# Kernel optimization log

Measured on AMD Instinct MI355X. Metric: run time of the kernel, lower is better.

## Reference

```python
import jax, jax.numpy as jnp
import numpy as np

B, S, IN, OUT = 8, 2048, 4096, 4096
SPARSE_FRACTION = 0.9
ALPHA = 0.3


def setup_inputs() -> dict:
    key = jax.random.key(0)
    k1, k2, k3 = jax.random.split(key, 3)
    total = IN * OUT
    target_nz = int(total * (1.0 - SPARSE_FRACTION))          # nonzeros after rigl step
    num_drop = int(ALPHA * target_nz)                          # = mask.sum() - target_nz
    # kaiming_uniform_(a=sqrt(5)) -> bound = 1/sqrt(fan_in)
    bound = 1.0 / np.sqrt(IN)
    weight = jax.random.uniform(k1, (OUT, IN), minval=-bound, maxval=bound, dtype=jnp.float32)
    x = jax.random.normal(k2, (B, S, IN), dtype=jnp.float32)
    dense_grad = jax.random.normal(k3, (OUT, IN), dtype=jnp.float32) * 0.01
    # mask starts with target_nz + num_drop nonzeros so the drop/grow path runs
    rng = np.random.default_rng(0)
    idx = rng.permutation(total)[: target_nz + num_drop]
    m = np.zeros(total, dtype=bool)
    m[idx] = True
    mask = jnp.asarray(m.reshape(OUT, IN))
    return {"x": x, "weight": weight, "dense_grad": dense_grad, "mask": mask, "num_drop": num_drop}


def _rigl_mask(weight, dense_grad, mask, num_drop):
    # RigL sparse-to-sparse update: drop smallest-|w|, grow largest-|grad| among masked-out slots.
    flat = mask.reshape(-1)
    if num_drop > 0:  # num_drop is a static Python int
        wmag = jnp.abs(weight).reshape(-1)
        _, drop_idx = jax.lax.top_k(-wmag, num_drop)           # smallest magnitudes
        flat = flat.at[drop_idx].set(False)
        gmag = jnp.abs(dense_grad).reshape(-1)
        grow_scores = jnp.where(flat, -jnp.inf, gmag)          # only grow where mask == 0
        _, grow_idx = jax.lax.top_k(grow_scores, num_drop)
        flat = flat.at[grow_idx].set(True)
    return flat.reshape(mask.shape)


def reference(x, weight, dense_grad, mask, num_drop):
    new_mask = _rigl_mask(weight, dense_grad, mask, num_drop)
    masked_weight = weight * new_mask.astype(weight.dtype)     # [OUT, IN]
    # F.linear: y = x @ W^T
    return jnp.einsum('bsi,oi->bso', x, masked_weight)
```

## Files before the change

### kernel.cpp

```cpp
#include <hip/hip_runtime.h>
#include <hip/hip_bf16.h>

#define M_TOT 16384
#define N_TOT 4096
#define K_TOT 4096
#define NELEM 16777216

typedef __attribute__((ext_vector_type(8))) short bf16x8;
typedef __attribute__((ext_vector_type(4))) float f32x4;

#define AS1 __attribute__((address_space(1)))
#define AS3 __attribute__((address_space(3)))

struct SelState {
  unsigned long long prefix;
  unsigned long long thr;
  unsigned int k_rem;
  unsigned int done;
  unsigned int active;
};

struct Ctl {
  unsigned long long pcount;
  unsigned int mask_is_byte;
  unsigned int cand_n;
  SelState d;
  SelState g;
};

__device__ Ctl g_ctl;
__device__ unsigned int g_hist[4096];
__device__ unsigned char g_elig[NELEM];
__device__ unsigned short g_wb[NELEM];
__device__ unsigned short g_xb[(size_t)M_TOT * K_TOT];
__device__ unsigned long long g_cand[NELEM];

__device__ __forceinline__ unsigned short f2bf(float f) {
  unsigned int u = __float_as_uint(f);
  unsigned int r = (u + 0x7FFFu + ((u >> 16) & 1u)) >> 16;
  return (unsigned short)r;
}

__device__ __forceinline__ unsigned long long key_drop_bits(unsigned int fb, int i) {
  unsigned int b = fb & 0x7FFFFFFFu;
  return (((unsigned long long)b) << 24) | (unsigned int)i;
}
__device__ __forceinline__ unsigned long long key_grow_bits(unsigned int fb, int i) {
  unsigned int b = ~(fb & 0x7FFFFFFFu);
  return (((unsigned long long)b) << 24) | (unsigned int)i;
}

__global__ void ctl_reset() {
  int t = threadIdx.x;
  if (t == 0) { g_ctl.pcount = 0ull; g_ctl.cand_n = 0u; }
  for (int i = t; i < 4096; i += 256) g_hist[i] = 0;
}

__global__ void mask_popcnt(const unsigned int* mw) {
  const int NW = NELEM / 4;
  unsigned int s = 0;
  for (int i = blockIdx.x * blockDim.x + threadIdx.x; i < NW; i += gridDim.x * blockDim.x)
    s += __popc(mw[i]);
  for (int off = 32; off > 0; off >>= 1) s += __shfl_down(s, off, 64);
  if ((threadIdx.x & 63) == 0)
    atomicAdd((unsigned long long*)&g_ctl.pcount, (unsigned long long)s);
}

__global__ void sel_init(const int* ndp) {
  unsigned int k = (unsigned int)ndp[0];
  g_ctl.mask_is_byte = (g_ctl.pcount > 1200000ull) ? 1u : 0u;
  SelState s;
  s.prefix = 0ull; s.thr = 0ull; s.k_rem = k;
  s.done = (k == 0u) ? 1u : 0u;
  s.active = (k > 0u) ? 1u : 0u;
  g_ctl.d = s;
  g_ctl.g = s;
}

template <int SEL>
__global__ __launch_bounds__(256) void hist_pass(const float* __restrict__ src, int shift, int nbits) {
  SelState& st = SEL ? g_ctl.g : g_ctl.d;
  if (st.done) return;
  __shared__ unsigned int lh[4096];
  const int nb = 1 << nbits;
  for (int i = threadIdx.x; i < nb; i += blockDim.x) lh[i] = 0;
  __syncthreads();
  const unsigned long long pref = st.prefix;
  const int N4 = NELEM / 4;
  for (int q = blockIdx.x * blockDim.x + threadIdx.x; q < N4; q += gridDim.x * blockDim.x) {
    float4 v = ((const float4*)src)[q];
    float fv[4] = {v.x, v.y, v.z, v.w};
    unsigned char ev[4] = {1, 1, 1, 1};
    if (SEL) {
      uchar4 e4 = ((const uchar4*)g_elig)[q];
      ev[0] = e4.x; ev[1] = e4.y; ev[2] = e4.z; ev[3] = e4.w;
    }
#pragma unroll
    for (int j = 0; j < 4; ++j) {
      if (SEL && !ev[j]) continue;
      int i = q * 4 + j;
      unsigned int fb = __float_as_uint(fv[j]);
      unsigned long long key = SEL ? key_grow_bits(fb, i) : key_drop_bits(fb, i);
      if ((key >> (shift + nbits)) == pref)
        atomicAdd(&lh[(unsigned int)(key >> shift) & (unsigned int)(nb - 1)], 1u);
    }
  }
  __syncthreads();
  for (int i = threadIdx.x; i < nb; i += blockDim.x)
    if (lh[i]) atomicAdd(&g_hist[i], lh[i]);
}

#define CCAP 4096
template <int SEL>
__global__ __launch_bounds__(256) void compact_pass(const float* __restrict__ src) {
  SelState& st = SEL ? g_ctl.g : g_ctl.d;
  if (st.done) return;
  __shared__ unsigned long long lk[CCAP];
  __shared__ unsigned int ln;
  __shared__ unsigned int gbase;
  if (threadIdx.x == 0) ln = 0;
  __syncthreads();
  const unsigned long long pref = st.prefix;
  const int N4 = NELEM / 4;
  for (int q = blockIdx.x * blockDim.x + threadIdx.x; q < N4; q += gridDim.x * blockDim.x) {
    float4 v = ((const float4*)src)[q];
    float fv[4] = {v.x, v.y, v.z, v.w};
    unsigned char ev[4] = {1, 1, 1, 1};
    if (SEL) {
      uchar4 e4 = ((const uchar4*)g_elig)[q];
      ev[0] = e4.x; ev[1] = e4.y; ev[2] = e4.z; ev[3] = e4.w;
    }
#pragma unroll
    for (int j = 0; j < 4; ++j) {
      if (SEL && !ev[j]) continue;
      int i = q * 4 + j;
      unsigned int fb = __float_as_uint(fv[j]);
      unsigned long long key = SEL ? key_grow_bits(fb, i) : key_drop_bits(fb, i);
      if ((key >> 44) == pref) {
        unsigned int slot = atomicAdd(&ln, 1u);
        if (slot < CCAP) {
          lk[slot] = key;
        } else {
          unsigned int gb = atomicAdd(&g_ctl.cand_n, 1u);
          g_cand[gb] = key;
        }
      }
    }
  }
  __syncthreads();
  unsigned int n = ln < CCAP ? ln : CCAP;
  if (threadIdx.x == 0) gbase = atomicAdd(&g_ctl.cand_n, n);
  __syncthreads();
  for (unsigned int i = threadIdx.x; i < n; i += blockDim.x)
    g_cand[gbase + i] = lk[i];
}

template <int SEL>
__global__ __launch_bounds__(256) void hist_cand(int shift, int nbits) {
  SelState& st = SEL ? g_ctl.g : g_ctl.d;
  if (st.done) return;
  __shared__ unsigned int lh[4096];
  const int nb = 1 << nbits;
  for (int i = threadIdx.x; i < nb; i += blockDim.x) lh[i] = 0;
  __syncthreads();
  const unsigned long long pref = st.prefix;
  const unsigned int n = g_ctl.cand_n;
  for (unsigned int i = blockIdx.x * blockDim.x + threadIdx.x; i < n; i += gridDim.x * blockDim.x) {
    unsigned long long key = g_cand[i];
    if ((key >> (shift + nbits)) == pref)
      atomicAdd(&lh[(unsigned int)(key >> shift) & (unsigned int)(nb - 1)], 1u);
  }
  __syncthreads();
  for (int i = threadIdx.x; i < nb; i += blockDim.x)
    if (lh[i]) atomicAdd(&g_hist[i], lh[i]);
}

template <int SEL>
__global__ void select_pass(int shift, int nbits) {
  SelState& st = SEL ? g_ctl.g : g_ctl.d;
  if (st.done) return;
  __shared__ unsigned int sc[256];
  __shared__ int tgt;
  const int nb = 1 << nbits;
  const int per = (nb + 255) / 256;
  const int t = threadIdx.x;
  unsigned int s = 0;
  for (int j = 0; j < per; ++j) {
    int b = t * per + j;
    if (b < nb) s += g_hist[b];
  }
  sc[t] = s;
  __syncthreads();
  for (int off = 1; off < 256; off <<= 1) {
    unsigned int v = (t >= off) ? sc[t - off] : 0u;
    __syncthreads();
    sc[t] += v;
    __syncthreads();
  }
  const unsigned int k = st.k_rem;
  const unsigned int cum = sc[t];
  const unsigned int before = cum - s;
  if (before < k && k <= cum) tgt = t;
  __syncthreads();
  if (t == tgt) {
    unsigned int c = before;
    for (int j = 0; j < per; ++j) {
      int b = t * per + j;
      unsigned int h = (b < nb) ? g_hist[b] : 0u;
      if (c + h >= k) {
        unsigned long long np = (st.prefix << nbits) | (unsigned long long)(unsigned int)b;
        st.prefix = np;
        st.k_rem = k - c;
        st.thr = ((np + 1ull) << shift) - 1ull;
        if (k - c == h) st.done = 1;
        break;
      }
      c += h;
    }
  }
  __syncthreads();
  for (int b = t; b < nb; b += 256) g_hist[b] = 0;
}

__global__ __launch_bounds__(256) void build_elig(const float* __restrict__ w, const void* maskp) {
  if (blockIdx.x == 0 && threadIdx.x == 0) g_ctl.cand_n = 0u;
  int q = blockIdx.x * blockDim.x + threadIdx.x;
  if (q >= NELEM / 4) return;
  float4 wv = ((const float4*)w)[q];
  float fv[4] = {wv.x, wv.y, wv.z, wv.w};
  unsigned char m[4];
  if (g_ctl.mask_is_byte) {
    uchar4 m4 = ((const uchar4*)maskp)[q];
    m[0] = m4.x; m[1] = m4.y; m[2] = m4.z; m[3] = m4.w;
  } else {
    int4 m4 = ((const int4*)maskp)[q];
    m[0] = m4.x != 0; m[1] = m4.y != 0; m[2] = m4.z != 0; m[3] = m4.w != 0;
  }
  const bool act = g_ctl.d.active;
  const unsigned long long thr = g_ctl.d.thr;
  uchar4 e;
  unsigned char ev[4];
#pragma unroll
  for (int j = 0; j < 4; ++j) {
    int i = q * 4 + j;
    bool dropped = act && (key_drop_bits(__float_as_uint(fv[j]), i) <= thr);
    ev[j] = (!m[j] || dropped) ? 1 : 0;
  }
  e.x = ev[0]; e.y = ev[1]; e.z = ev[2]; e.w = ev[3];
  ((uchar4*)g_elig)[q] = e;
}

__global__ __launch_bounds__(256) void build_wb(const float* __restrict__ w, const float* __restrict__ gr) {
  int q = blockIdx.x * blockDim.x + threadIdx.x;
  if (q >= NELEM / 4) return;
  float4 wv = ((const float4*)w)[q];
  float4 gv = ((const float4*)gr)[q];
  float wf[4] = {wv.x, wv.y, wv.z, wv.w};
  float gf[4] = {gv.x, gv.y, gv.z, gv.w};
  uchar4 e4 = ((const uchar4*)g_elig)[q];
  unsigned char ev[4] = {e4.x, e4.y, e4.z, e4.w};
  const bool act = g_ctl.g.active;
  const unsigned long long thr = g_ctl.g.thr;
  ushort4 o;
  unsigned short ov[4];
#pragma unroll
  for (int j = 0; j < 4; ++j) {
    int i = q * 4 + j;
    bool keep;
    if (!ev[j]) keep = true;
    else keep = act && (key_grow_bits(__float_as_uint(gf[j]), i) <= thr);
    ov[j] = keep ? f2bf(wf[j]) : (unsigned short)0;
  }
  o.x = ov[0]; o.y = ov[1]; o.z = ov[2]; o.w = ov[3];
  ((ushort4*)g_wb)[q] = o;
}

__global__ __launch_bounds__(256) void convert_x(const float* __restrict__ x) {
  int i = blockIdx.x * blockDim.x + threadIdx.x;
  float4 v = ((const float4*)x)[i];
  ushort4 o;
  o.x = f2bf(v.x); o.y = f2bf(v.y); o.z = f2bf(v.z); o.w = f2bf(v.w);
  ((ushort4*)g_xb)[i] = o;
}

#define BM2 256
#define BN2 256
#define BK2 64
#define NT2 (K_TOT / BK2)
#define BUFB (256 * 128)

__global__ __launch_bounds__(512, 2) void gemm_kernel(float* __restrict__ out) {
  __shared__ unsigned short As[2][BM2][BK2];
  __shared__ unsigned short Bs[2][BN2][BK2];
  const int tid = threadIdx.x;
  const int lane = tid & 63;
  const int w = tid >> 6;
  const int wm = w >> 2, wn = w & 3;

  const int orig = blockIdx.x;
  const int swz = (orig & 7) * 128 + (orig >> 3);
  const int gm0 = (swz >> 4) * BM2;
  const int gn0 = (swz & 15) * BN2;

  f32x4 acc[8][4];
#pragma unroll
  for (int i = 0; i < 8; ++i)
#pragma unroll
    for (int j = 0; j < 4; ++j) acc[i][j] = (f32x4){0.f, 0.f, 0.f, 0.f};

  const int sr = (w << 3) + (lane >> 3);
  const int sc = 8 * ((lane & 7) ^ (lane >> 3));
  const unsigned short* Agp = g_xb + (size_t)(gm0 + sr) * K_TOT + sc;
  const unsigned short* Bgp = g_wb + (size_t)(gn0 + sr) * K_TOT + sc;
  const int lr = (w << 3);

#define STAGE_A(tile, half) do {                                             \
    const int bi_ = (tile) & 1; const int kb_ = ((tile) & (NT2 - 1)) * BK2;  \
    __builtin_amdgcn_global_load_lds(                                        \
        (const AS1 void*)(Agp + (size_t)((half) * 128) * K_TOT + kb_),       \
        (AS3 void*)(&As[bi_][(half) * 128 + lr][0]), 16, 0, 0);              \
    __builtin_amdgcn_global_load_lds(                                        \
        (const AS1 void*)(Agp + (size_t)((half) * 128 + 64) * K_TOT + kb_),  \
        (AS3 void*)(&As[bi_][(half) * 128 + 64 + lr][0]), 16, 0, 0);         \
  } while (0)
#define STAGE_B(tile, half) do {                                             \
    const int bi_ = (tile) & 1; const int kb_ = ((tile) & (NT2 - 1)) * BK2;  \
    __builtin_amdgcn_global_load_lds(                                        \
        (const AS1 void*)(Bgp + (size_t)((half) * 128) * K_TOT + kb_),       \
        (AS3 void*)(&Bs[bi_][(half) * 128 + lr][0]), 16, 0, 0);              \
    __builtin_amdgcn_global_load_lds(                                        \
        (const AS1 void*)(Bgp + (size_t)((half) * 128 + 64) * K_TOT + kb_),  \
        (AS3 void*)(&Bs[bi_][(half) * 128 + 64 + lr][0]), 16, 0, 0);         \
  } while (0)

  const int r16 = lane & 15;
  const int kcb = (lane >> 4) << 4;
  const int xv = (r16 & 7) << 4;
  const char* Ab0 = (const char*)&As[0][wm * 128][0];
  const char* Bb0 = (const char*)&Bs[0][wn * 64][0];

  bf16x8 pA[4][2], pB0[2][2], pB1[2][2];

#define LD_A(qm, bi) do {                                                     \
    const char* ab_ = Ab0 + (bi) * BUFB + ((qm) * 64 + r16) * 128;            \
    _Pragma("unroll") for (int mi = 0; mi < 4; ++mi)                          \
      _Pragma("unroll") for (int sk = 0; sk < 2; ++sk)                        \
        pA[mi][sk] = *(const bf16x8*)(ab_ + mi * 16 * 128 +                   \
                                      ((sk * 64 + kcb) ^ xv));                \
  } while (0)
#define LD_B(P, qn, bi) do {                                                  \
    const char* bb_ = Bb0 + (bi) * BUFB + ((qn) * 32 + r16) * 128;            \
    _Pragma("unroll") for (int nf = 0; nf < 2; ++nf)                          \
      _Pragma("unroll") for (int sk = 0; sk < 2; ++sk)                        \
        P[nf][sk] = *(const bf16x8*)(bb_ + nf * 16 * 128 +                    \
                                     ((sk * 64 + kcb) ^ xv));                 \
  } while (0)
#define MFMA_Q(qm, qn, P) do {                                                \
    __builtin_amdgcn_s_setprio(1);                                            \
    _Pragma("unroll") for (int mi = 0; mi < 4; ++mi)                          \
      _Pragma("unroll") for (int nf = 0; nf < 2; ++nf)                        \
        _Pragma("unroll") for (int sk = 0; sk < 2; ++sk)                      \
          acc[(qm) * 4 + mi][(qn) * 2 + nf] =                                 \
              __builtin_amdgcn_mfma_f32_16x16x32_bf16(                        \
                  pA[mi][sk], P[nf][sk], acc[(qm) * 4 + mi][(qn) * 2 + nf],   \
                  0, 0, 0);                                                   \
    __builtin_amdgcn_s_setprio(0);                                            \
  } while (0)
#define BAR() __builtin_amdgcn_s_barrier()
#define WLG() asm volatile("s_waitcnt lgkmcnt(0)" ::: "memory")
#define WVM6() asm volatile("s_waitcnt vmcnt(6)" ::: "memory")

  STAGE_A(0, 0); STAGE_A(0, 1); STAGE_B(0, 0); STAGE_B(0, 1);
  STAGE_B(1, 0); STAGE_B(1, 1); STAGE_A(1, 0);
  WVM6();
  BAR();

  for (int it = 0; it < NT2 / 2; ++it) {
    const int T = 2 * it;
    LD_A(0, 0); LD_B(pB0, 0, 0); LD_B(pB1, 1, 0);
    STAGE_A(T + 1, 1);
    BAR(); WLG();
    MFMA_Q(0, 0, pB0);
    BAR();
    STAGE_B(T + 2, 0);
    BAR();
    MFMA_Q(0, 1, pB1);
    BAR();
    LD_A(1, 0);
    STAGE_B(T + 2, 1);
    BAR(); WLG();
    MFMA_Q(1, 1, pB1);
    BAR();
    STAGE_A(T + 2, 0);
    BAR();
    MFMA_Q(1, 0, pB0);
    WVM6();
    BAR();
    LD_A(0, 1); LD_B(pB0, 0, 1); LD_B(pB1, 1, 1);
    STAGE_A(T + 2, 1);
    BAR(); WLG();
    MFMA_Q(0, 0, pB0);
    BAR();
    STAGE_B(T + 3, 0);
    BAR();
    MFMA_Q(0, 1, pB1);
    BAR();
    LD_A(1, 1);
    STAGE_B(T + 3, 1);
    BAR(); WLG();
    MFMA_Q(1, 1, pB1);
    BAR();
    STAGE_A(T + 3, 0);
    BAR();
    MFMA_Q(1, 0, pB0);
    WVM6();
    BAR();
  }

  const int cm0 = gm0 + wm * 128 + (lane >> 4) * 4;
  const int cn0 = gn0 + wn * 64 + (lane & 15);
#pragma unroll
  for (int mi = 0; mi < 8; ++mi)
#pragma unroll
    for (int nf = 0; nf < 4; ++nf)
#pragma unroll
      for (int r = 0; r < 4; ++r)
        out[(size_t)(cm0 + mi * 16 + r) * N_TOT + cn0 + nf * 16] = acc[mi][nf][r];
}

extern "C" void kernel_launch(void* const* d_in, const int* in_sizes, int n_in,
                              void* d_out, int out_size, void* d_ws, size_t ws_size,
                              hipStream_t stream) {
  const float* x  = (const float*)d_in[0];
  const float* wt = (const float*)d_in[1];
  const float* gr = (const float*)d_in[2];
  const void*  mk = d_in[3];
  const int*   nd = (const int*)d_in[4];
  (void)d_ws; (void)ws_size; (void)in_sizes; (void)n_in; (void)out_size;

  ctl_reset<<<1, 256, 0, stream>>>();
  mask_popcnt<<<512, 256, 0, stream>>>((const unsigned int*)mk);
  sel_init<<<1, 1, 0, stream>>>(nd);

  const int shifts[5] = {44, 32, 24, 12, 0};
  const int nbits[5]  = {12, 12, 8, 12, 12};

  hist_pass<0><<<1024, 256, 0, stream>>>(wt, shifts[0], nbits[0]);
  select_pass<0><<<1, 256, 0, stream>>>(shifts[0], nbits[0]);
  compact_pass<0><<<1024, 256, 0, stream>>>(wt);
  for (int p = 1; p < 5; ++p) {
    hist_cand<0><<<256, 256, 0, stream>>>(shifts[p], nbits[p]);
    select_pass<0><<<1, 256, 0, stream>>>(shifts[p], nbits[p]);
  }
  build_elig<<<NELEM / 4 / 256, 256, 0, stream>>>(wt, mk);
  hist_pass<1><<<1024, 256, 0, stream>>>(gr, shifts[0], nbits[0]);
  select_pass<1><<<1, 256, 0, stream>>>(shifts[0], nbits[0]);
  compact_pass<1><<<1024, 256, 0, stream>>>(gr);
  for (int p = 1; p < 5; ++p) {
    hist_cand<1><<<256, 256, 0, stream>>>(shifts[p], nbits[p]);
    select_pass<1><<<1, 256, 0, stream>>>(shifts[p], nbits[p]);
  }
  build_wb<<<NELEM / 4 / 256, 256, 0, stream>>>(wt, gr);
  convert_x<<<(M_TOT * K_TOT / 4) / 256, 256, 0, stream>>>(x);
  gemm_kernel<<<1024, 512, 0, stream>>>((float*)d_out);
}
```

Before: 1.011 ms.

## Stage GEMM epilogue through LDS for float4 stores and split B fragment loads

```diff
diff --git a/kernel.cpp b/kernel.cpp
--- a/kernel.cpp
+++ b/kernel.cpp
@@ -290,8 +290,9 @@
 #define BUFB (256 * 128)
 
 __global__ __launch_bounds__(512, 2) void gemm_kernel(float* __restrict__ out) {
-  __shared__ unsigned short As[2][BM2][BK2];
-  __shared__ unsigned short Bs[2][BN2][BK2];
+  __shared__ __align__(16) char smem[131072];
+  unsigned short* Asb = (unsigned short*)smem;
+  unsigned short* Bsb = (unsigned short*)(smem + 65536);
   const int tid = threadIdx.x;
   const int lane = tid & 63;
   const int w = tid >> 6;
@@ -318,26 +319,30 @@
     const int bi_ = (tile) & 1; const int kb_ = ((tile) & (NT2 - 1)) * BK2;  \
     __builtin_amdgcn_global_load_lds(                                        \
         (const AS1 void*)(Agp + (size_t)((half) * 128) * K_TOT + kb_),       \
-        (AS3 void*)(&As[bi_][(half) * 128 + lr][0]), 16, 0, 0);              \
+        (AS3 void*)(Asb + (size_t)bi_ * (BM2 * BK2) +                        \
+                    ((half) * 128 + lr) * BK2), 16, 0, 0);                   \
     __builtin_amdgcn_global_load_lds(                                        \
         (const AS1 void*)(Agp + (size_t)((half) * 128 + 64) * K_TOT + kb_),  \
-        (AS3 void*)(&As[bi_][(half) * 128 + 64 + lr][0]), 16, 0, 0);         \
+        (AS3 void*)(Asb + (size_t)bi_ * (BM2 * BK2) +                        \
+                    ((half) * 128 + 64 + lr) * BK2), 16, 0, 0);              \
   } while (0)
 #define STAGE_B(tile, half) do {                                             \
     const int bi_ = (tile) & 1; const int kb_ = ((tile) & (NT2 - 1)) * BK2;  \
     __builtin_amdgcn_global_load_lds(                                        \
         (const AS1 void*)(Bgp + (size_t)((half) * 128) * K_TOT + kb_),       \
-        (AS3 void*)(&Bs[bi_][(half) * 128 + lr][0]), 16, 0, 0);              \
+        (AS3 void*)(Bsb + (size_t)bi_ * (BN2 * BK2) +                        \
+                    ((half) * 128 + lr) * BK2), 16, 0, 0);                   \
     __builtin_amdgcn_global_load_lds(                                        \
         (const AS1 void*)(Bgp + (size_t)((half) * 128 + 64) * K_TOT + kb_),  \
-        (AS3 void*)(&Bs[bi_][(half) * 128 + 64 + lr][0]), 16, 0, 0);         \
+        (AS3 void*)(Bsb + (size_t)bi_ * (BN2 * BK2) +                        \
+                    ((half) * 128 + 64 + lr) * BK2), 16, 0, 0);              \
   } while (0)
 
   const int r16 = lane & 15;
   const int kcb = (lane >> 4) << 4;
   const int xv = (r16 & 7) << 4;
-  const char* Ab0 = (const char*)&As[0][wm * 128][0];
-  const char* Bb0 = (const char*)&Bs[0][wn * 64][0];
+  const char* Ab0 = (const char*)(Asb + wm * 128 * BK2);
+  const char* Bb0 = (const char*)(Bsb + wn * 64 * BK2);
 
   bf16x8 pA[4][2], pB0[2][2], pB1[2][2];
 
@@ -368,6 +373,7 @@
   } while (0)
 #define BAR() __builtin_amdgcn_s_barrier()
 #define WLG() asm volatile("s_waitcnt lgkmcnt(0)" ::: "memory")
+#define WLG8() asm volatile("s_waitcnt lgkmcnt(8)" ::: "memory")
 #define WVM6() asm volatile("s_waitcnt vmcnt(6)" ::: "memory")
 
   STAGE_A(0, 0); STAGE_A(0, 1); STAGE_B(0, 0); STAGE_B(0, 1);
@@ -377,13 +383,15 @@
 
   for (int it = 0; it < NT2 / 2; ++it) {
     const int T = 2 * it;
-    LD_A(0, 0); LD_B(pB0, 0, 0); LD_B(pB1, 1, 0);
+    LD_A(0, 0); LD_B(pB0, 0, 0);
     STAGE_A(T + 1, 1);
+    WLG8();
     BAR(); WLG();
     MFMA_Q(0, 0, pB0);
     BAR();
+    LD_B(pB1, 1, 0);
     STAGE_B(T + 2, 0);
-    BAR();
+    BAR(); WLG();
     MFMA_Q(0, 1, pB1);
     BAR();
     LD_A(1, 0);
@@ -396,13 +404,15 @@
     MFMA_Q(1, 0, pB0);
     WVM6();
     BAR();
-    LD_A(0, 1); LD_B(pB0, 0, 1); LD_B(pB1, 1, 1);
+    LD_A(0, 1); LD_B(pB0, 0, 1);
     STAGE_A(T + 2, 1);
+    WLG8();
     BAR(); WLG();
     MFMA_Q(0, 0, pB0);
     BAR();
+    LD_B(pB1, 1, 1);
     STAGE_B(T + 3, 0);
-    BAR();
+    BAR(); WLG();
     MFMA_Q(0, 1, pB1);
     BAR();
     LD_A(1, 1);
@@ -417,15 +427,30 @@
     BAR();
   }
 
-  const int cm0 = gm0 + wm * 128 + (lane >> 4) * 4;
-  const int cn0 = gn0 + wn * 64 + (lane & 15);
-#pragma unroll
-  for (int mi = 0; mi < 8; ++mi)
-#pragma unroll
-    for (int nf = 0; nf < 4; ++nf)
-#pragma unroll
-      for (int r = 0; r < 4; ++r)
-        out[(size_t)(cm0 + mi * 16 + r) * N_TOT + cn0 + nf * 16] = acc[mi][nf][r];
+  float* lf = (float*)smem;
+#pragma unroll
+  for (int Q = 0; Q < 4; ++Q) {
+    __syncthreads();
+#pragma unroll
+    for (int m2 = 0; m2 < 2; ++m2) {
+      const int rl0 = (wm * 2 + m2) * 16 + (lane >> 4) * 4;
+#pragma unroll
+      for (int nf = 0; nf < 4; ++nf) {
+        const int col = wn * 64 + nf * 16 + (lane & 15);
+#pragma unroll
+        for (int r = 0; r < 4; ++r)
+          lf[(rl0 + r) * 260 + col] = acc[Q * 2 + m2][nf][r];
+      }
+    }
+    __syncthreads();
+#pragma unroll
+    for (int i2 = 0; i2 < 8; ++i2) {
+      const int rl = w * 8 + i2;
+      const int grow = (rl >> 5) * 128 + (Q * 2 + ((rl >> 4) & 1)) * 16 + (rl & 15);
+      *(float4*)&out[(size_t)(gm0 + grow) * N_TOT + gn0 + lane * 4] =
+          *(const float4*)&lf[rl * 260 + lane * 4];
+    }
+  }
 }
 
 extern "C" void kernel_launch(void* const* d_in, const int* in_sizes, int n_in,
```

Measured after the change: 882.2 us. -12.8%, faster.
